# Kernel optimization log

Measured on AMD Instinct MI355X. Metric: run time of the kernel, lower is better.

Reference implementation:

```python
import jax, jax.numpy as jnp
import numpy as np

KAPPA = -1.0          # negative curvature (Poincare ball, c = 1)
EPS = 1e-10
N, D_IN, D_OUT = 8192, 512, 512


def _artan_k(x):
    sc = np.sqrt(-KAPPA)
    return jnp.arctanh(jnp.clip(sc * x, -1.0 + 1e-7, 1.0 - 1e-7)) / sc


def _tan_k(x):
    sc = np.sqrt(-KAPPA)
    return jnp.tanh(sc * x) / sc


def _clamp_abs(x, eps=EPS):
    return jnp.where(x >= 0, 1.0, -1.0) * jnp.maximum(jnp.abs(x), eps)


def _norm(x):
    # stable last-dim L2 norm, clamped away from zero
    return jnp.sqrt(jnp.maximum(jnp.sum(x * x, axis=-1, keepdims=True), EPS * EPS))


def mobius_matvec(W, x):
    # geoopt-style Mobius matrix-vector product: scale x@W so that the
    # gyro-norm matches tan_k((|mx|/|x|) * artan_k(|x|))
    x_norm = _norm(x)                       # [N,1]
    mx = x @ W                              # [N,D_out]
    mx_norm = _norm(mx)
    res = _tan_k(mx_norm / x_norm * _artan_k(x_norm)) * (mx / mx_norm)
    return jnp.where(mx_norm <= EPS, 0.0, res)


def mobius_scalar_mul(r, x):
    x_norm = _norm(x)
    return _tan_k(r * _artan_k(x_norm)) * (x / x_norm)


def weighted_midpoint_lincomb(A, X):
    # weighted Frechet-mean-like midpoint with lincomb=True (geoopt semantics):
    # gamma_i = lambda_x = 2 / (1 + kappa * |x_i|^2)
    gamma = jnp.maximum(2.0 / (1.0 + KAPPA * jnp.sum(X * X, axis=-1, keepdims=True)), 1e-15)  # [N,1]
    denom = _clamp_abs(A @ (gamma - 1.0))   # [N,1]  (sum_j A_ij (gamma_j - 1))
    nom = A @ (gamma * X)                   # [N,D]  (sum_j A_ij gamma_j x_j)  -- GEMM, no NxNxD temp
    two_mean = nom / denom
    sq = jnp.sum(two_mean * two_mean, axis=-1, keepdims=True)
    a_mean = two_mean / (1.0 + jnp.sqrt(jnp.maximum(1.0 + KAPPA * sq, EPS)))
    alpha = jnp.sum(A, axis=-1, keepdims=True)   # lincomb: Mobius-scale by total weight
    return mobius_scalar_mul(alpha, a_mean)


def logmap0(x):
    xn = _norm(x)
    return _artan_k(xn) * x / xn


def expmap0(u):
    un = _norm(u)
    return _tan_k(un) * u / un


def setup_inputs() -> dict:
    key = jax.random.key(0)
    k1, k2, k3 = jax.random.split(key, 3)
    # node embeddings well inside the Poincare ball (|x| ~ 0.02)
    X = jax.random.normal(k1, (N, D_IN), dtype=jnp.float32) * 0.001
    # dense nonnegative normalized adjacency (rows sum ~ 0.5)
    A_hat = jax.random.uniform(k2, (N, N), dtype=jnp.float32) / N
    W = jax.random.normal(k3, (D_IN, D_OUT), dtype=jnp.float32) * 0.01
    return {"X": X, "A_hat": A_hat, "W": W}


def reference(X, A_hat, W):
    XW = mobius_matvec(W, X)                     # Mobius linear layer
    AXW = weighted_midpoint_lincomb(A_hat, XW)   # adjacency-weighted midpoint aggregation
    return expmap0(jax.nn.relu(logmap0(AXW)))    # sigma = exp0(relu(log0(.)))
```

## Files before the change

kernel.cpp:

```cpp
#include <hip/hip_runtime.h>


#define NR 8192
#define DD 512

typedef unsigned int u32;
typedef unsigned short u16;
typedef __attribute__((ext_vector_type(8))) short bf16x8;
typedef __attribute__((ext_vector_type(4))) float f32x4;

__device__ __forceinline__ u16 f2bf(float f) {
  u32 u = __float_as_uint(f);
  u32 r = u + 0x7FFFu + ((u >> 16) & 1u);
  return (u16)(r >> 16);
}

__device__ __forceinline__ u32 cvtpk(float lo, float hi) {
  u32 r;
  asm("v_cvt_pk_bf16_f32 %0, %1, %2" : "=v"(r) : "v"(lo), "v"(hi));
  return r;
}

__device__ __forceinline__ void gload16(const void* g, void* l) {
  __builtin_amdgcn_global_load_lds(
      (const __attribute__((address_space(1))) u32*)g,
      (__attribute__((address_space(3))) u32*)l, 16, 0, 0);
}

__device__ __forceinline__ float wred(float v) {
  #pragma unroll
  for (int off = 32; off; off >>= 1) v += __shfl_xor(v, off, 64);
  return v;
}

__global__ __launch_bounds__(256) void conv_wt(const float* __restrict__ W,
                                               u16* __restrict__ Wt) {
  const int idx = blockIdx.x * 256 + threadIdx.x;
  const int n  = idx >> 6;
  const int k0 = (idx & 63) * 8;
  u32 r[4];
  #pragma unroll
  for (int j = 0; j < 4; ++j) {
    float lo = W[(size_t)(k0 + 2*j    ) * DD + n];
    float hi = W[(size_t)(k0 + 2*j + 1) * DD + n];
    r[j] = (u32)f2bf(lo) | ((u32)f2bf(hi) << 16);
  }
  const int dst = n * DD + ((idx & 63) >> 2) * 32 + (((idx & 3) ^ (n & 3)) * 8);
  *(uint4*)(Wt + dst) = *(const uint4*)r;
}

template <int DOSUM>
__global__ __launch_bounds__(512, 2) void gemm_big(
    const float* __restrict__ Af, const u16* __restrict__ Bt,
    const u16* __restrict__ g1bf,
    float* __restrict__ C0, float* __restrict__ Cext,
    float* __restrict__ denp, float* __restrict__ alp,
    int M, int K, int kchunk, int nkc) {
  __shared__ __align__(16) float ldsA[2][4096];
  __shared__ __align__(16) u16   ldsB[2][16384];
  __shared__ __align__(16) u16   ldsG[2048];

  const int bid = blockIdx.x;
  int mt, kc;
  if (nkc == 1) { mt = bid; kc = 0; }
  else { kc = (bid & 7) >> 1; mt = ((bid >> 3) << 1) | (bid & 1); }

  const int t = threadIdx.x;
  const int lane = t & 63, w = t >> 6;
  const int wm = w >> 2, wn = w & 3;
  const int m0 = mt * 128;
  const int kbeg = kc * kchunk;
  const int lr = lane & 15, lk = lane >> 4, lx = lr & 7;

  const int Rb   = t >> 3;
  const int scol = ((t & 7) ^ (Rb & 7)) << 2;
  const float* gA0 = Af + (size_t)(m0 + Rb) * K + kbeg + scol;

  const u16* gB = Bt + (size_t)(t >> 2) * K + kbeg + (t & 3) * 8;

  f32x4 acc[4][8];
  #pragma unroll
  for (int i = 0; i < 4; ++i)
    #pragma unroll
    for (int j = 0; j < 8; ++j) acc[i][j] = (f32x4){0.f, 0.f, 0.f, 0.f};
  f32x4 accS[4];
  #pragma unroll
  for (int i = 0; i < 4; ++i) accS[i] = (f32x4){0.f, 0.f, 0.f, 0.f};

  const int nT = kchunk / 32;

  if (DOSUM && w < 4) gload16(g1bf + kbeg + t * 8, &ldsG[t * 8]);
  #pragma unroll
  for (int j = 0; j < 2; ++j)
    gload16(gA0 + (size_t)j * 64 * K, &ldsA[0][t * 4 + j * 2048]);
  #pragma unroll
  for (int j = 0; j < 4; ++j)
    gload16(gB + (size_t)j * 128 * K, &ldsB[0][t * 8 + j * 4096]);
  __syncthreads();

  for (int tt = 0; tt < nT; ++tt) {
    const int cur = tt & 1, nxt = cur ^ 1;
    if (tt + 1 < nT) {
      const int ko = (tt + 1) * 32;
      #pragma unroll
      for (int j = 0; j < 2; ++j)
        gload16(gA0 + ko + (size_t)j * 64 * K, &ldsA[nxt][t * 4 + j * 2048]);
      #pragma unroll
      for (int j = 0; j < 4; ++j)
        gload16(gB + ko + (size_t)j * 128 * K, &ldsB[nxt][t * 8 + j * 4096]);
    }
    bf16x8 af[4], bv[8];
    #pragma unroll
    for (int i = 0; i < 4; ++i) {
      const int rbase = (wm * 64 + i * 16 + lr) * 32;
      f32x4 lo = *(const f32x4*)&ldsA[cur][rbase + (((2*lk    ) ^ lx) << 2)];
      f32x4 hi = *(const f32x4*)&ldsA[cur][rbase + (((2*lk + 1) ^ lx) << 2)];
      union { u32 u[4]; bf16x8 v; } pk;
      pk.u[0] = cvtpk(lo.x, lo.y); pk.u[1] = cvtpk(lo.z, lo.w);
      pk.u[2] = cvtpk(hi.x, hi.y); pk.u[3] = cvtpk(hi.z, hi.w);
      af[i] = pk.v;
    }
    #pragma unroll
    for (int i = 0; i < 8; ++i) {
      const int rb = (wn * 128 + i * 16 + lr) * 32 + ((lk ^ (lr & 3)) << 3);
      bv[i] = *(const bf16x8*)&ldsB[cur][rb];
    }
    #pragma unroll
    for (int mi = 0; mi < 4; ++mi)
      #pragma unroll
      for (int ni = 0; ni < 8; ++ni)
        acc[mi][ni] = __builtin_amdgcn_mfma_f32_16x16x32_bf16(
            af[mi], bv[ni], acc[mi][ni], 0, 0, 0);
    if (DOSUM && wn == 0) {
      bf16x8 gv;
      if (lr == 0) {
        gv = *(const bf16x8*)&ldsG[tt * 32 + lk * 8];
      } else {
        const short s = (lr == 1) ? (short)0x3F80 : (short)0;
        gv = (bf16x8){s, s, s, s, s, s, s, s};
      }
      #pragma unroll
      for (int i = 0; i < 4; ++i)
        accS[i] = __builtin_amdgcn_mfma_f32_16x16x32_bf16(
            af[i], gv, accS[i], 0, 0, 0);
    }
    __syncthreads();
  }

  if (DOSUM && wn == 0 && lr < 2) {
    float* dst = ((lr == 0) ? denp : alp) + (size_t)kc * M + m0 + wm * 64;
    #pragma unroll
    for (int i = 0; i < 4; ++i)
      #pragma unroll
      for (int v = 0; v < 4; ++v)
        dst[i * 16 + lk * 4 + v] = accS[i][v];
  }

  float* C = (kc == 0) ? C0 : (Cext + (size_t)(kc - 1) * M * DD);
  float* Cw = C + (size_t)(m0 + wm * 64 + lk * 4) * DD + wn * 128 + lr;
  #pragma unroll
  for (int mi = 0; mi < 4; ++mi)
    #pragma unroll
    for (int ni = 0; ni < 8; ++ni)
      #pragma unroll
      for (int v = 0; v < 4; ++v)
        Cw[(size_t)(mi * 16 + v) * DD + ni * 16] = acc[mi][ni][v];
}

__global__ __launch_bounds__(256) void rowstats(const float* __restrict__ X,
                                                const float* __restrict__ mx,
                                                float* __restrict__ fg,
                                                u16* __restrict__ g1bf) {
  const int row  = (blockIdx.x << 2) + (threadIdx.x >> 6);
  const int lane = threadIdx.x & 63;
  const float* xr = X  + (size_t)row * DD + lane * 8;
  const float* mr = mx + (size_t)row * DD + lane * 8;
  float4 a0 = *(const float4*)xr, a1 = *(const float4*)(xr + 4);
  float4 b0 = *(const float4*)mr, b1 = *(const float4*)(mr + 4);
  float sx = a0.x*a0.x + a0.y*a0.y + a0.z*a0.z + a0.w*a0.w
           + a1.x*a1.x + a1.y*a1.y + a1.z*a1.z + a1.w*a1.w;
  float sm = b0.x*b0.x + b0.y*b0.y + b0.z*b0.z + b0.w*b0.w
           + b1.x*b1.x + b1.y*b1.y + b1.z*b1.z + b1.w*b1.w;
  sx = wred(sx); sm = wred(sm);
  if (lane == 0) {
    float xn  = sqrtf(fmaxf(sx, 1e-20f));
    float mxn = sqrtf(fmaxf(sm, 1e-20f));
    float at  = atanhf(fminf(xn, 0.9999999f));
    float t_  = tanhf(mxn / xn * at);
    bool  z   = (mxn <= 1e-10f);
    float factor = z ? 0.f : t_ / mxn;
    float xwsq   = z ? 0.f : t_ * t_ * (sm / (mxn * mxn));
    float g = 2.f / (1.f - xwsq);
    g = fmaxf(g, 1e-15f);
    fg[row] = factor * g;
    g1bf[row] = f2bf(g - 1.f);
  }
}

__global__ __launch_bounds__(256) void build_bt(const float* __restrict__ mx,
                                                const float* __restrict__ fg,
                                                u16* __restrict__ Bt) {
  __shared__ float tile[64][65];
  const int j0 = blockIdx.x * 64, d0 = blockIdx.y * 64;
  const int t = threadIdx.x;
  const int r0 = t >> 4, c4 = (t & 15) * 4;
  #pragma unroll
  for (int p = 0; p < 4; ++p) {
    const int r = r0 + p * 16;
    const float s = fg[j0 + r];
    float4 v = *(const float4*)&mx[(size_t)(j0 + r) * DD + d0 + c4];
    tile[r][c4 + 0] = s * v.x; tile[r][c4 + 1] = s * v.y;
    tile[r][c4 + 2] = s * v.z; tile[r][c4 + 3] = s * v.w;
  }
  __syncthreads();
  const int dr = t >> 2, jc = (t & 3) * 16;
  u32 r[8];
  #pragma unroll
  for (int u = 0; u < 8; ++u) {
    float lo = tile[jc + 2 * u][dr];
    float hi = tile[jc + 2 * u + 1][dr];
    r[u] = (u32)f2bf(lo) | ((u32)f2bf(hi) << 16);
  }
  const int s0 = (jc >> 3) & 3;
  const int px = dr & 3;
  u32* rowp = (u32*)(Bt + (size_t)(d0 + dr) * NR + j0 + (jc & 32));
  *(uint4*)(rowp + ((s0 ^ px) * 4))       = *(const uint4*)&r[0];
  *(uint4*)(rowp + (((s0 + 1) ^ px) * 4)) = *(const uint4*)&r[4];
}

__global__ __launch_bounds__(256) void epilogue(const float* __restrict__ P0,
                                                const float* __restrict__ P1,
                                                const float* __restrict__ P2,
                                                const float* __restrict__ P3,
                                                const float* __restrict__ denp,
                                                const float* __restrict__ alp,
                                                float* __restrict__ out) {
  const int row  = (blockIdx.x << 2) + (threadIdx.x >> 6);
  const int lane = threadIdx.x & 63;
  const size_t ro = (size_t)row * DD + lane * 8;
  float4 n0 = *(const float4*)(P0 + ro), n1 = *(const float4*)(P0 + ro + 4);
  float4 a, b;
  a = *(const float4*)(P1 + ro); b = *(const float4*)(P1 + ro + 4);
  n0.x += a.x; n0.y += a.y; n0.z += a.z; n0.w += a.w;
  n1.x += b.x; n1.y += b.y; n1.z += b.z; n1.w += b.w;
  a = *(const float4*)(P2 + ro); b = *(const float4*)(P2 + ro + 4);
  n0.x += a.x; n0.y += a.y; n0.z += a.z; n0.w += a.w;
  n1.x += b.x; n1.y += b.y; n1.z += b.z; n1.w += b.w;
  a = *(const float4*)(P3 + ro); b = *(const float4*)(P3 + ro + 4);
  n0.x += a.x; n0.y += a.y; n0.z += a.z; n0.w += a.w;
  n1.x += b.x; n1.y += b.y; n1.z += b.z; n1.w += b.w;

  float de = 0.f, alpha = 0.f;
  #pragma unroll
  for (int kc = 0; kc < 4; ++kc) {
    de    += denp[kc * NR + row];
    alpha += alp [kc * NR + row];
  }
  de = (de >= 0.f ? 1.f : -1.f) * fmaxf(fabsf(de), 1e-10f);

  float v[8] = {n0.x / de, n0.y / de, n0.z / de, n0.w / de,
                n1.x / de, n1.y / de, n1.z / de, n1.w / de};
  float sq = 0.f;
  #pragma unroll
  for (int j = 0; j < 8; ++j) sq += v[j] * v[j];
  sq = wred(sq);
  float s1 = 1.f + sqrtf(fmaxf(1.f - sq, 1e-10f));
  float an = sqrtf(fmaxf(sq / (s1 * s1), 1e-20f));
  float t2 = tanhf(alpha * atanhf(fminf(an, 0.9999999f)));
  float f2 = t2 / (an * s1);
  float xsq = f2 * f2 * sq;
  float xn = sqrtf(fmaxf(xsq, 1e-20f));
  float lf = atanhf(fminf(xn, 0.9999999f)) / xn;
  float u[8]; float us = 0.f;
  #pragma unroll
  for (int j = 0; j < 8; ++j) {
    u[j] = fmaxf(lf * f2 * v[j], 0.f);
    us += u[j] * u[j];
  }
  us = wred(us);
  float un = sqrtf(fmaxf(us, 1e-20f));
  float ef = tanhf(un) / un;
  float o[8];
  #pragma unroll
  for (int j = 0; j < 8; ++j) o[j] = ef * u[j];
  float* orow = out + (size_t)row * DD + lane * 8;
  *(float4*)orow       = (float4){o[0], o[1], o[2], o[3]};
  *(float4*)(orow + 4) = (float4){o[4], o[5], o[6], o[7]};
}

extern "C" void kernel_launch(void* const* d_in, const int* in_sizes, int n_in,
                              void* d_out, int out_size, void* d_ws, size_t ws_size,
                              hipStream_t stream) {
  const float* X = (const float*)d_in[0];
  const float* A = (const float*)d_in[1];
  const float* W = (const float*)d_in[2];
  float* out = (float*)d_out;
  char* ws = (char*)d_ws;

  float* mx   = (float*)(ws);
  float* Pext = (float*)(ws + 16777216);
  u16*   Bt   = (u16*)(ws + 67108864);
  u16*   Wt   = (u16*)(ws + 75497472);
  float* fg   = (float*)(ws + 76021760);
  u16*   g1bf = (u16*)(ws + 76054528);
  float* denp = (float*)(ws + 76087296);
  float* alp  = (float*)(ws + 76218368);

  const size_t MNf = (size_t)NR * DD;

  conv_wt<<<128, 256, 0, stream>>>(W, Wt);
  gemm_big<0><<<64, 512, 0, stream>>>(X, Wt, g1bf, mx, mx, denp, alp,
                                      NR, DD, DD, 1);
  rowstats<<<2048, 256, 0, stream>>>(X, mx, fg, g1bf);
  build_bt<<<dim3(128, 8), 256, 0, stream>>>(mx, fg, Bt);
  gemm_big<1><<<256, 512, 0, stream>>>(A, Bt, g1bf, mx, Pext, denp, alp,
                                       NR, NR, NR / 4, 4);
  epilogue<<<2048, 256, 0, stream>>>(mx, Pext, Pext + MNf, Pext + 2 * MNf,
                                     denp, alp, out);
}
```

Before: 220.7 us.

## Prefetch two K-tiles ahead with fine-grained vmcnt waits in GEMM main loop

Restructures the double-buffered GEMM loop so that two tiles are staged up front. The next-next tile is issued into the current buffer right after its fragments have been read into registers and a barrier has passed. It replaces the full __syncthreads with explicit s_waitcnt vmcnt(6)/lgkmcnt(0) plus s_barrier and sched_barriers, which lets global loads overlap MFMA work across a deeper window. The risk is correctness around the waitcnt counts, especially if the DOSUM ldsG load also counts toward vmcnt. The pinned scheduling may also limit compiler interleaving.

```diff
diff --git a/kernel.cpp b/kernel.cpp
--- a/kernel.cpp
+++ b/kernel.cpp
@@ -78,6 +78,16 @@
 
   const u16* gB = Bt + (size_t)(t >> 2) * K + kbeg + (t & 3) * 8;
 
+  auto stage = [&](int buf, int kt) {
+    const int ko = kt * 32;
+    #pragma unroll
+    for (int j = 0; j < 2; ++j)
+      gload16(gA0 + ko + (size_t)j * 64 * K, &ldsA[buf][t * 4 + j * 2048]);
+    #pragma unroll
+    for (int j = 0; j < 4; ++j)
+      gload16(gB + ko + (size_t)j * 128 * K, &ldsB[buf][t * 8 + j * 4096]);
+  };
+
   f32x4 acc[4][8];
   #pragma unroll
   for (int i = 0; i < 4; ++i)
@@ -90,25 +100,14 @@
   const int nT = kchunk / 32;
 
   if (DOSUM && w < 4) gload16(g1bf + kbeg + t * 8, &ldsG[t * 8]);
-  #pragma unroll
-  for (int j = 0; j < 2; ++j)
-    gload16(gA0 + (size_t)j * 64 * K, &ldsA[0][t * 4 + j * 2048]);
-  #pragma unroll
-  for (int j = 0; j < 4; ++j)
-    gload16(gB + (size_t)j * 128 * K, &ldsB[0][t * 8 + j * 4096]);
-  __syncthreads();
-
+  stage(0, 0);
+  stage(1, 1);
+  asm volatile("s_waitcnt vmcnt(6)" ::: "memory");
+  __builtin_amdgcn_s_barrier();
+  __builtin_amdgcn_sched_barrier(0);
+
+  int cur = 0;
   for (int tt = 0; tt < nT; ++tt) {
-    const int cur = tt & 1, nxt = cur ^ 1;
-    if (tt + 1 < nT) {
-      const int ko = (tt + 1) * 32;
-      #pragma unroll
-      for (int j = 0; j < 2; ++j)
-        gload16(gA0 + ko + (size_t)j * 64 * K, &ldsA[nxt][t * 4 + j * 2048]);
-      #pragma unroll
-      for (int j = 0; j < 4; ++j)
-        gload16(gB + ko + (size_t)j * 128 * K, &ldsB[nxt][t * 8 + j * 4096]);
-    }
     bf16x8 af[4], bv[8];
     #pragma unroll
     for (int i = 0; i < 4; ++i) {
@@ -125,6 +124,20 @@
       const int rb = (wn * 128 + i * 16 + lr) * 32 + ((lk ^ (lr & 3)) << 3);
       bv[i] = *(const bf16x8*)&ldsB[cur][rb];
     }
+    bf16x8 gv;
+    if (DOSUM && wn == 0) {
+      if (lr == 0) {
+        gv = *(const bf16x8*)&ldsG[tt * 32 + lk * 8];
+      } else {
+        const short s = (lr == 1) ? (short)0x3F80 : (short)0;
+        gv = (bf16x8){s, s, s, s, s, s, s, s};
+      }
+    }
+    asm volatile("s_waitcnt lgkmcnt(0)" ::: "memory");
+    __builtin_amdgcn_s_barrier();
+    __builtin_amdgcn_sched_barrier(0);
+    if (tt + 2 < nT) stage(cur, tt + 2);
+    __builtin_amdgcn_sched_barrier(0);
     #pragma unroll
     for (int mi = 0; mi < 4; ++mi)
       #pragma unroll
@@ -132,19 +145,22 @@
         acc[mi][ni] = __builtin_amdgcn_mfma_f32_16x16x32_bf16(
             af[mi], bv[ni], acc[mi][ni], 0, 0, 0);
     if (DOSUM && wn == 0) {
-      bf16x8 gv;
-      if (lr == 0) {
-        gv = *(const bf16x8*)&ldsG[tt * 32 + lk * 8];
-      } else {
-        const short s = (lr == 1) ? (short)0x3F80 : (short)0;
-        gv = (bf16x8){s, s, s, s, s, s, s, s};
-      }
       #pragma unroll
       for (int i = 0; i < 4; ++i)
         accS[i] = __builtin_amdgcn_mfma_f32_16x16x32_bf16(
             af[i], gv, accS[i], 0, 0, 0);
     }
-    __syncthreads();
+    if (tt + 1 < nT) {
+      __builtin_amdgcn_sched_barrier(0);
+      if (tt + 2 < nT) {
+        asm volatile("s_waitcnt vmcnt(6)" ::: "memory");
+      } else {
+        asm volatile("s_waitcnt vmcnt(0)" ::: "memory");
+      }
+      __builtin_amdgcn_s_barrier();
+      __builtin_amdgcn_sched_barrier(0);
+    }
+    cur ^= 1;
   }
 
   if (DOSUM && wn == 0 && lr < 2) {
```

After: 201.1 us. 8.9% less time.
